# Kernel optimization log

Hardware: AMD Instinct MI355X
Metric: run time of the kernel (lower is better)

Reference implementation:

```python
import jax, jax.numpy as jnp
import numpy as np

N, E, IN_F, H1, F1, H2, F2, OUT_F = 50000, 800000, 128, 4, 32, 1, 64, 2
NEG_SLOPE = 0.2  # PyG GATConv default


def setup_inputs() -> dict:
    key = jax.random.key(0)
    ks = jax.random.split(key, 10)
    p = lambda k, shp: jax.random.normal(k, shp, jnp.float32) * 0.1
    return {
        "x": jax.random.normal(ks[0], (N, IN_F), jnp.float32),
        "edge_index": jax.random.randint(ks[1], (2, E), 0, N),
        "W1": p(ks[2], (IN_F, H1 * F1)),
        "att_s1": p(ks[3], (H1, F1)),
        "att_d1": p(ks[4], (H1, F1)),
        "b1": jnp.zeros((H1 * F1,), jnp.float32),
        "W2": p(ks[5], (H1 * F1, H2 * F2)),
        "att_s2": p(ks[6], (H2, F2)),
        "att_d2": p(ks[7], (H2, F2)),
        "b2": jnp.zeros((F2,), jnp.float32),
        "Wl": p(ks[8], (F2, OUT_F)),
        "bl": jnp.zeros((OUT_F,), jnp.float32),
    }


def _gat_conv(x, src, dst, W, att_s, att_d, bias, concat):
    # PyG GATConv: per-head linear, leaky-relu attention logits,
    # segment-softmax over incoming edges of each dst, scatter-add aggregate.
    n = x.shape[0]
    H, F = att_s.shape
    h = (x @ W).reshape(n, H, F)                        # [N, H, F]
    a_s = jnp.einsum('nhf,hf->nh', h, att_s)            # [N, H]
    a_d = jnp.einsum('nhf,hf->nh', h, att_d)
    logits = jax.nn.leaky_relu(a_s[src] + a_d[dst], NEG_SLOPE)  # [Etot, H]
    m = jax.ops.segment_max(logits, dst, num_segments=n)
    e = jnp.exp(logits - m[dst])
    denom = jax.ops.segment_sum(e, dst, num_segments=n)
    alpha = e / denom[dst]                              # segment softmax
    msg = h[src] * alpha[:, :, None]                    # [Etot, H, F]
    out = jax.ops.segment_sum(msg, dst, num_segments=n)  # [N, H, F]
    out = out.reshape(n, H * F) if concat else out.mean(axis=1)
    return out + bias


def reference(x, edge_index, W1, att_s1, att_d1, b1, W2, att_s2, att_d2, b2, Wl, bl):
    n = x.shape[0]
    loops = jnp.arange(n, dtype=edge_index.dtype)       # add_self_loops=True
    src = jnp.concatenate([edge_index[0], loops])
    dst = jnp.concatenate([edge_index[1], loops])
    h = jax.nn.elu(_gat_conv(x, src, dst, W1, att_s1, att_d1, b1, True))
    h = jax.nn.elu(_gat_conv(h, src, dst, W2, att_s2, att_d2, b2, False))
    pooled = h.sum(axis=0, keepdims=True)               # global_add_pool, batch=0
    out = pooled @ Wl + bl
    return pooled, out
```

## Files before the change

kernel.cpp:

```cpp
#include <hip/hip_runtime.h>

#define N_NODES 50000
#define N_EDGES 800000
#define NB 196
#define P1_BLOCKS 256
#define EPB 3125
#define BH_SIZE (NB * P1_BLOCKS)
#define GEMM_BLOCKS ((N_NODES + 63) / 64)
#define AGG_BLOCKS (N_NODES / 4)
#define EBS_CAP 5120

__device__ __forceinline__ float lrelu(float x) { return fmaxf(x, 0.2f * x); }
__device__ __forceinline__ float elu(float x) { return x > 0.f ? x : __expf(x) - 1.f; }

typedef float f32x2 __attribute__((ext_vector_type(2)));
typedef float f32x4v __attribute__((ext_vector_type(4)));
typedef short bf16x8 __attribute__((ext_vector_type(8)));

__device__ __forceinline__ unsigned f2bf_rn(float x) {
  unsigned u = __float_as_uint(x);
  return (u + 0x7fffu + ((u >> 16) & 1u)) >> 16;
}
__device__ __forceinline__ unsigned pack2bf(float a, float b) {
  return f2bf_rn(a) | (f2bf_rn(b) << 16);
}
__device__ __forceinline__ uint4 pack8bf(const float* v) {
  uint4 o;
  o.x = pack2bf(v[0], v[1]); o.y = pack2bf(v[2], v[3]);
  o.z = pack2bf(v[4], v[5]); o.w = pack2bf(v[6], v[7]);
  return o;
}

__device__ __forceinline__ int block_excl_scan(int v, int* total_out) {
  int lane = threadIdx.x & 63;
  int wid = threadIdx.x >> 6;
  int x = v;
#pragma unroll
  for (int off = 1; off < 64; off <<= 1) {
    int u = __shfl_up(x, off);
    if (lane >= off) x += u;
  }
  __shared__ int wsum[4];
  if (lane == 63) wsum[wid] = x;
  __syncthreads();
  int add = 0;
#pragma unroll
  for (int k = 0; k < 4; ++k)
    if (k < wid) add += wsum[k];
  if (total_out) *total_out = wsum[0] + wsum[1] + wsum[2] + wsum[3];
  return x + add - v;
}

__global__ __launch_bounds__(256) void setup_hist_kernel(
    const int* __restrict__ ei, int* __restrict__ bh,
    const float* __restrict__ W1, const float* __restrict__ atts1, const float* __restrict__ attd1,
    const float* __restrict__ W2, const float* __restrict__ atts2, const float* __restrict__ attd2,
    uint4* __restrict__ Wpk1, uint4* __restrict__ Wpk2, float* __restrict__ pooled) {
  __shared__ int cnt[NB];
  int bid = blockIdx.x;
  if (bid >= 2) {
    for (int t = threadIdx.x; t < NB; t += 256) cnt[t] = 0;
    __syncthreads();
    int start = (bid - 2) * EPB;
    for (int i = start + threadIdx.x; i < start + EPB; i += 256)
      atomicAdd(&cnt[ei[N_EDGES + i] >> 8], 1);
    __syncthreads();
    for (int t = threadIdx.x; t < NB; t += 256)
      bh[t * P1_BLOCKS + (bid - 2)] = cnt[t];
    return;
  }
  if (bid == 0) {
    for (int s = threadIdx.x; s < 4 * 9 * 64; s += 256) {
      int l = s & 63, sf = s >> 6;
      int f = sf % 9, ks = sf / 9;
      int colb = f * 16 + (l & 15);
      int kb = ks * 32 + ((l >> 4) << 3);
      float v[8];
      if (colb < 128) {
#pragma unroll
        for (int j = 0; j < 8; ++j) v[j] = W1[(kb + j) * 128 + colb];
      } else if (colb < 136) {
        int cc = colb - 128;
        const float* at = (cc < 4) ? atts1 : attd1;
        int h = cc & 3;
#pragma unroll
        for (int j = 0; j < 8; ++j) {
          float s2 = 0.f;
          for (int q = 0; q < 32; ++q) s2 += W1[(kb + j) * 128 + h * 32 + q] * at[h * 32 + q];
          v[j] = s2;
        }
      } else {
#pragma unroll
        for (int j = 0; j < 8; ++j) v[j] = 0.f;
      }
      Wpk1[s] = pack8bf(v);
    }
  } else {
    for (int s = threadIdx.x; s < 4 * 5 * 64; s += 256) {
      int l = s & 63, sf = s >> 6;
      int f = sf % 5, ks = sf / 5;
      int colb = f * 16 + (l & 15);
      int kb = ks * 32 + ((l >> 4) << 3);
      float v[8];
      if (colb < 64) {
#pragma unroll
        for (int j = 0; j < 8; ++j) v[j] = W2[(kb + j) * 64 + colb];
      } else if (colb < 66) {
        const float* at = (colb == 64) ? atts2 : attd2;
#pragma unroll
        for (int j = 0; j < 8; ++j) {
          float s2 = 0.f;
          for (int q = 0; q < 64; ++q) s2 += W2[(kb + j) * 64 + q] * at[q];
          v[j] = s2;
        }
      } else {
#pragma unroll
        for (int j = 0; j < 8; ++j) v[j] = 0.f;
      }
      Wpk2[s] = pack8bf(v);
    }
    for (int i = threadIdx.x; i < 64 * 64; i += 256) pooled[i] = 0.f;
  }
}

template <int NF, bool ABF16>
__device__ __forceinline__ void mfma_gemm_body(int bx, const void* __restrict__ Ap,
                                               const uint4* __restrict__ Wpk,
                                               unsigned* __restrict__ Yb,
                                               float* __restrict__ as_out, float* __restrict__ ad_out) {
  __shared__ unsigned short Xs[64 * 136];
  __shared__ uint4 Ws[NF * 64];
  int t = threadIdx.x;
  int rbase = bx * 64;
  if constexpr (ABF16) {
    const uint4* A4 = (const uint4*)Ap;
#pragma unroll
    for (int p = 0; p < 4; ++p) {
      int i = p * 256 + t;
      int row = i >> 4, q = i & 15;
      int gr = rbase + row; if (gr > N_NODES - 1) gr = N_NODES - 1;
      *(uint4*)&Xs[row * 136 + q * 8] = A4[gr * 16 + q];
    }
  } else {
    const float4* A4 = (const float4*)Ap;
#pragma unroll
    for (int p = 0; p < 8; ++p) {
      int i = p * 256 + t;
      int row = i >> 5, q = i & 31;
      int gr = rbase + row; if (gr > N_NODES - 1) gr = N_NODES - 1;
      float4 v = A4[gr * 32 + q];
      *(uint2*)&Xs[row * 136 + q * 4] = make_uint2(pack2bf(v.x, v.y), pack2bf(v.z, v.w));
    }
  }

  int l = t & 63, wv = t >> 6;
  int lc = l & 15, lk = l >> 4;
  f32x4v acc[NF];
#pragma unroll
  for (int f = 0; f < NF; ++f) acc[f] = (f32x4v){0.f, 0.f, 0.f, 0.f};
  const unsigned short* ap = &Xs[(wv * 16 + lc) * 136 + lk * 8];
#pragma unroll
  for (int ks = 0; ks < 4; ++ks) {
    for (int i = t; i < NF * 64; i += 256) Ws[i] = Wpk[ks * NF * 64 + i];
    __syncthreads();
    bf16x8 a = *(const bf16x8*)(ap + ks * 32);
#pragma unroll
    for (int f = 0; f < NF; ++f) {
      bf16x8 b = *(const bf16x8*)&Ws[f * 64 + l];
      acc[f] = __builtin_amdgcn_mfma_f32_16x16x32_bf16(a, b, acc[f], 0, 0, 0);
    }
    if (ks < 3) __syncthreads();
  }

  constexpr int NCF = NF - 1;
#pragma unroll
  for (int reg = 0; reg < 4; ++reg) {
    int row = rbase + wv * 16 + lk * 4 + reg;
    bool rok = row < N_NODES;
    float av = acc[NCF][reg];
    if (rok) {
      if constexpr (NF == 9) {
        if (lc < 4) as_out[row * 4 + lc] = av;
        else if (lc < 8) ad_out[row * 4 + lc - 4] = av;
      } else {
        if (lc == 0) as_out[row] = av;
        else if (lc == 1) ad_out[row] = av;
      }
    }
    unsigned words[NCF];
#pragma unroll
    for (int f = 0; f < NCF; ++f) {
      float v = acc[f][reg];
      float n1 = __shfl_xor(v, 1);
      unsigned pk = (unsigned)__builtin_amdgcn_cvt_pk_fp8_f32(v, n1, 0, false);
      unsigned pk2 = (unsigned)__shfl_xor((int)pk, 2);
      words[f] = (pk & 0xffffu) | (pk2 << 16);
    }
    if (rok && (lc & 3) == 0) {
#pragma unroll
      for (int f = 0; f < NCF; ++f)
        Yb[row * (NCF * 4) + f * 4 + (lc >> 2)] = words[f];
    }
  }
}

__global__ __launch_bounds__(256) void gemm128_scan_kernel(
    const float* __restrict__ x, const uint4* __restrict__ Wpk1,
    unsigned* __restrict__ h1b, float* __restrict__ as1, float* __restrict__ ad1,
    const int* __restrict__ bh, int* __restrict__ bhP, int* __restrict__ blocksum) {
  if (blockIdx.x < GEMM_BLOCKS) {
    mfma_gemm_body<9, false>(blockIdx.x, x, Wpk1, h1b, as1, ad1);
  } else {
    int b = blockIdx.x - GEMM_BLOCKS;
    int g = b * 256 + threadIdx.x;
    int v = bh[g];
    int total;
    int ex = block_excl_scan(v, &total);
    bhP[g] = ex;
    if (threadIdx.x == 0) blocksum[b] = total;
  }
}

__global__ __launch_bounds__(256) void gemm64_kernel(const uint4* __restrict__ h1eb,
                                                     const uint4* __restrict__ Wpk2,
                                                     unsigned* __restrict__ h2b,
                                                     float* __restrict__ as2, float* __restrict__ ad2) {
  mfma_gemm_body<5, true>(blockIdx.x, h1eb, Wpk2, h2b, as2, ad2);
}

__global__ __launch_bounds__(256) void scatter1_kernel(const int* __restrict__ ei, const int* __restrict__ bhP,
                                                       const int* __restrict__ blocksum, unsigned* __restrict__ eb) {
  __shared__ int cur[NB];
  __shared__ int boff[NB];
  int t = threadIdx.x;
  for (int i = t; i < NB; i += 256) cur[i] = 0;
  {
    int v = (t < NB) ? blocksum[t] : 0;
    int ex = block_excl_scan(v, nullptr);
    if (t < NB) boff[t] = ex;
  }
  __syncthreads();
  int start = blockIdx.x * EPB;
  for (int i = start + t; i < start + EPB; i += 256) {
    int dst = ei[N_EDGES + i];
    int src = ei[i];
    int bin = dst >> 8;
    int r = atomicAdd(&cur[bin], 1);
    int idx = bin * P1_BLOCKS + blockIdx.x;
    int pos = bhP[idx] + boff[bin] + r;
    eb[pos] = (unsigned)src | ((unsigned)(dst & 255) << 16);
  }
}

__global__ __launch_bounds__(256) void bucket_csr_kernel(const unsigned* __restrict__ eb,
                                                         const int* __restrict__ blocksum,
                                                         int* __restrict__ rowptrF, int* __restrict__ col) {
  __shared__ unsigned ebs[EBS_CAP];
  __shared__ int cnt[256];
  __shared__ int basel[256];
  __shared__ int cur[256];
  __shared__ int sse[2];
  int b = blockIdx.x;
  int t = threadIdx.x;
  {
    int v = (t < NB) ? blocksum[t] : 0;
    int ex0 = block_excl_scan(v, nullptr);
    if (t == b) sse[0] = ex0;
    if (t == b + 1) sse[1] = ex0;
  }
  cnt[t] = 0;
  cur[t] = 0;
  __syncthreads();
  int start = sse[0];
  int end = (b == NB - 1) ? N_EDGES : sse[1];
  int m = end - start;
  bool fits = (m <= EBS_CAP);
  for (int i = t; i < m; i += 256) {
    unsigned e = eb[start + i];
    if (fits) ebs[i] = e;
    atomicAdd(&cnt[e >> 16], 1);
  }
  __syncthreads();
  int ex = block_excl_scan(cnt[t], nullptr);
  basel[t] = start + ex;
  int g = b * 256 + t;
  if (g < N_NODES) rowptrF[g] = start + ex;
  if (g == N_NODES) rowptrF[N_NODES] = N_EDGES;
  __syncthreads();
  for (int i = t; i < m; i += 256) {
    unsigned e = fits ? ebs[i] : eb[start + i];
    int d8 = e >> 16;
    int r = atomicAdd(&cur[d8], 1);
    col[basel[d8] + r] = (int)(e & 0xffffu);
  }
}

__global__ __launch_bounds__(256) void agg1_kernel(const uint2* __restrict__ h1f8, const int* __restrict__ rowptr,
                                                   const int* __restrict__ col, const float* __restrict__ as1,
                                                   const float* __restrict__ ad1, const float4* __restrict__ b1v,
                                                   uint4* __restrict__ h1eb4) {
  int n = (blockIdx.x * 256 + threadIdx.x) >> 6;
  int lane = threadIdx.x & 63;
  int slot = lane >> 4;
  int fo = lane & 15;
  int h = fo >> 2;
  int beg = rowptr[n], end = rowptr[n + 1];
  float adh = ad1[n * 4 + h];

  f32x2 acc2[4];
#pragma unroll
  for (int j = 0; j < 4; ++j) acc2[j] = (f32x2){0.f, 0.f};
  float esum = 0.f;

#define ACC_EDGE1(E)                                               \
  {                                                                \
    int src = col[E];                                              \
    float a = __expf(lrelu(as1[src * 4 + h] + adh));               \
    esum += a;                                                     \
    f32x2 av = {a, a};                                             \
    uint2 uu = h1f8[src * 16 + fo];                                \
    f32x2 p0 = __builtin_amdgcn_cvt_pk_f32_fp8(uu.x, false);       \
    f32x2 p1 = __builtin_amdgcn_cvt_pk_f32_fp8(uu.x, true);        \
    f32x2 p2 = __builtin_amdgcn_cvt_pk_f32_fp8(uu.y, false);       \
    f32x2 p3 = __builtin_amdgcn_cvt_pk_f32_fp8(uu.y, true);       \
    acc2[0] += av * p0; acc2[1] += av * p1;                        \
    acc2[2] += av * p2; acc2[3] += av * p3;                        \
  }

  int i = beg;
  for (; i + 16 <= end; i += 16) {
#pragma unroll
    for (int u = 0; u < 4; ++u) ACC_EDGE1(i + u * 4 + slot);
  }
  for (; i + 4 <= end; i += 4) ACC_EDGE1(i + slot);
  int rem = end - i;
  if (slot < rem) ACC_EDGE1(i + slot);
#undef ACC_EDGE1
  if (slot == 0) {
    float a = __expf(lrelu(as1[n * 4 + h] + adh));
    esum += a;
    f32x2 av = {a, a};
    uint2 uu = h1f8[n * 16 + fo];
    f32x2 p0 = __builtin_amdgcn_cvt_pk_f32_fp8(uu.x, false);
    f32x2 p1 = __builtin_amdgcn_cvt_pk_f32_fp8(uu.x, true);
    f32x2 p2 = __builtin_amdgcn_cvt_pk_f32_fp8(uu.y, false);
    f32x2 p3 = __builtin_amdgcn_cvt_pk_f32_fp8(uu.y, true);
    acc2[0] += av * p0; acc2[1] += av * p1;
    acc2[2] += av * p2; acc2[3] += av * p3;
  }
#pragma unroll
  for (int j = 0; j < 4; ++j) {
    acc2[j].x += __shfl_xor(acc2[j].x, 16);
    acc2[j].y += __shfl_xor(acc2[j].y, 16);
    acc2[j].x += __shfl_xor(acc2[j].x, 32);
    acc2[j].y += __shfl_xor(acc2[j].y, 32);
  }
  esum += __shfl_xor(esum, 16);
  esum += __shfl_xor(esum, 32);
  if (slot == 0) {
    float dsc = 1.f / esum;
    float4 b0 = b1v[fo * 2], b1 = b1v[fo * 2 + 1];
    float f0 = elu(acc2[0].x * dsc + b0.x), f1 = elu(acc2[0].y * dsc + b0.y);
    float f2 = elu(acc2[1].x * dsc + b0.z), f3 = elu(acc2[1].y * dsc + b0.w);
    float f4 = elu(acc2[2].x * dsc + b1.x), f5 = elu(acc2[2].y * dsc + b1.y);
    float f6 = elu(acc2[3].x * dsc + b1.z), f7 = elu(acc2[3].y * dsc + b1.w);
    uint4 o;
    o.x = pack2bf(f0, f1); o.y = pack2bf(f2, f3);
    o.z = pack2bf(f4, f5); o.w = pack2bf(f6, f7);
    h1eb4[n * 16 + fo] = o;
  }
}

__global__ __launch_bounds__(256) void agg2_kernel(const uint2* __restrict__ h2f8, const int* __restrict__ rowptr,
                                                   const int* __restrict__ col, const float* __restrict__ as2,
                                                   const float* __restrict__ ad2, const float4* __restrict__ b2v,
                                                   float* __restrict__ pooled) {
  __shared__ float red[4][64];
  int n = (blockIdx.x * 256 + threadIdx.x) >> 6;
  int lane = threadIdx.x & 63;
  int wid = threadIdx.x >> 6;
  int slot = lane >> 3;
  int fo = lane & 7;
  int beg = rowptr[n], end = rowptr[n + 1];
  float ad = ad2[n];

  f32x2 acc2[4];
#pragma unroll
  for (int j = 0; j < 4; ++j) acc2[j] = (f32x2){0.f, 0.f};
  float esum = 0.f;

#define ACC_EDGE2(E)                                               \
  {                                                                \
    int src = col[E];                                              \
    float a = __expf(lrelu(as2[src] + ad));                        \
    esum += a;                                                     \
    f32x2 av = {a, a};                                             \
    uint2 uu = h2f8[src * 8 + fo];                                 \
    f32x2 p0 = __builtin_amdgcn_cvt_pk_f32_fp8(uu.x, false);       \
    f32x2 p1 = __builtin_amdgcn_cvt_pk_f32_fp8(uu.x, true);        \
    f32x2 p2 = __builtin_amdgcn_cvt_pk_f32_fp8(uu.y, false);       \
    f32x2 p3 = __builtin_amdgcn_cvt_pk_f32_fp8(uu.y, true);       \
    acc2[0] += av * p0; acc2[1] += av * p1;                        \
    acc2[2] += av * p2; acc2[3] += av * p3;                        \
  }

  int i = beg;
  for (; i + 32 <= end; i += 32) {
#pragma unroll
    for (int u = 0; u < 4; ++u) ACC_EDGE2(i + u * 8 + slot);
  }
  for (; i + 8 <= end; i += 8) ACC_EDGE2(i + slot);
  int rem = end - i;
  if (slot < rem) ACC_EDGE2(i + slot);
#undef ACC_EDGE2
  if (slot == 0) {
    float a = __expf(lrelu(as2[n] + ad));
    esum += a;
    f32x2 av = {a, a};
    uint2 uu = h2f8[n * 8 + fo];
    f32x2 p0 = __builtin_amdgcn_cvt_pk_f32_fp8(uu.x, false);
    f32x2 p1 = __builtin_amdgcn_cvt_pk_f32_fp8(uu.x, true);
    f32x2 p2 = __builtin_amdgcn_cvt_pk_f32_fp8(uu.y, false);
    f32x2 p3 = __builtin_amdgcn_cvt_pk_f32_fp8(uu.y, true);
    acc2[0] += av * p0; acc2[1] += av * p1;
    acc2[2] += av * p2; acc2[3] += av * p3;
  }
#pragma unroll
  for (int j = 0; j < 4; ++j) {
#pragma unroll
    for (int off = 8; off <= 32; off <<= 1) {
      acc2[j].x += __shfl_xor(acc2[j].x, off);
      acc2[j].y += __shfl_xor(acc2[j].y, off);
    }
  }
  esum += __shfl_xor(esum, 8);
  esum += __shfl_xor(esum, 16);
  esum += __shfl_xor(esum, 32);
  if (slot == 0) {
    float dsc = 1.f / esum;
    float4 b0 = b2v[fo * 2], b1 = b2v[fo * 2 + 1];
    red[wid][fo * 8 + 0] = elu(acc2[0].x * dsc + b0.x);
    red[wid][fo * 8 + 1] = elu(acc2[0].y * dsc + b0.y);
    red[wid][fo * 8 + 2] = elu(acc2[1].x * dsc + b0.z);
    red[wid][fo * 8 + 3] = elu(acc2[1].y * dsc + b0.w);
    red[wid][fo * 8 + 4] = elu(acc2[2].x * dsc + b1.x);
    red[wid][fo * 8 + 5] = elu(acc2[2].y * dsc + b1.y);
    red[wid][fo * 8 + 6] = elu(acc2[3].x * dsc + b1.z);
    red[wid][fo * 8 + 7] = elu(acc2[3].y * dsc + b1.w);
  }
  __syncthreads();
  if (threadIdx.x < 64) {
    float sum = red[0][threadIdx.x] + red[1][threadIdx.x] + red[2][threadIdx.x] + red[3][threadIdx.x];
    atomicAdd(&pooled[(blockIdx.x & 63) * 64 + threadIdx.x], sum);
  }
}

__global__ void final_kernel(const float* __restrict__ pooledS, const float* __restrict__ Wl,
                             const float* __restrict__ bl, float* __restrict__ out) {
  __shared__ float p[64];
  int t = threadIdx.x;
  float v = 0.f;
  for (int k = 0; k < 64; ++k) v += pooledS[k * 64 + t];
  p[t] = v;
  out[t] = v;
  __syncthreads();
  if (t < 2) {
    float s = bl[t];
    for (int k = 0; k < 64; ++k) s += p[k] * Wl[k * 2 + t];
    out[64 + t] = s;
  }
}

extern "C" void kernel_launch(void* const* d_in, const int* in_sizes, int n_in,
                              void* d_out, int out_size, void* d_ws, size_t ws_size,
                              hipStream_t stream) {
  (void)in_sizes; (void)n_in; (void)out_size; (void)ws_size;
  const float* x     = (const float*)d_in[0];
  const int*   ei    = (const int*)d_in[1];
  const float* W1    = (const float*)d_in[2];
  const float* atts1 = (const float*)d_in[3];
  const float* attd1 = (const float*)d_in[4];
  const float* b1    = (const float*)d_in[5];
  const float* W2    = (const float*)d_in[6];
  const float* atts2 = (const float*)d_in[7];
  const float* attd2 = (const float*)d_in[8];
  const float* b2    = (const float*)d_in[9];
  const float* Wl    = (const float*)d_in[10];
  const float* bl    = (const float*)d_in[11];
  float* out = (float*)d_out;

  char* w = (char*)d_ws;
  unsigned* h1b  = (unsigned*)w; w += (size_t)N_NODES * 128;
  unsigned* h1eb = (unsigned*)w; w += (size_t)N_NODES * 128 * 2;
  unsigned* h2b  = (unsigned*)w; w += (size_t)N_NODES * 64;
  float* as1  = (float*)w; w += (size_t)N_NODES * 16;
  float* ad1  = (float*)w; w += (size_t)N_NODES * 16;
  float* as2  = (float*)w; w += (size_t)N_NODES * 4;
  float* ad2  = (float*)w; w += (size_t)N_NODES * 4;
  float* pooled = (float*)w; w += 64 * 64 * 4;
  uint4* Wpk1 = (uint4*)w; w += 4 * 9 * 64 * 16;
  uint4* Wpk2 = (uint4*)w; w += 4 * 5 * 64 * 16;
  int* rowptrF = (int*)w; w += (size_t)(N_NODES + 1) * 4 + 12;
  int* col    = (int*)w; w += (size_t)N_EDGES * 4;
  unsigned* eb = (unsigned*)w; w += (size_t)N_EDGES * 4;
  int* bh     = (int*)w; w += (size_t)BH_SIZE * 4;
  int* bhP    = (int*)w; w += (size_t)BH_SIZE * 4;
  int* blocksum = (int*)w; w += 256 * 4;

  setup_hist_kernel<<<258, 256, 0, stream>>>(ei, bh, W1, atts1, attd1, W2, atts2, attd2,
                                             Wpk1, Wpk2, pooled);
  gemm128_scan_kernel<<<GEMM_BLOCKS + NB, 256, 0, stream>>>(x, Wpk1, h1b, as1, ad1, bh, bhP, blocksum);
  scatter1_kernel<<<P1_BLOCKS, 256, 0, stream>>>(ei, bhP, blocksum, eb);
  bucket_csr_kernel<<<NB, 256, 0, stream>>>(eb, blocksum, rowptrF, col);
  agg1_kernel<<<AGG_BLOCKS, 256, 0, stream>>>((const uint2*)h1b, rowptrF, col, as1, ad1,
                                              (const float4*)b1, (uint4*)h1eb);
  gemm64_kernel<<<GEMM_BLOCKS, 256, 0, stream>>>((const uint4*)h1eb, Wpk2, h2b, as2, ad2);
  agg2_kernel<<<AGG_BLOCKS, 256, 0, stream>>>((const uint2*)h2b, rowptrF, col, as2, ad2,
                                              (const float4*)b2, pooled);
  final_kernel<<<1, 64, 0, stream>>>(pooled, Wl, bl, out);
}
```

Measured before the change: 204.9 us.

## Fold histogram scan into scatter blocks and final reduction into agg2 last-block

Removes the separate scan pass and scatter kernel: each scatter block, co-launched with the first GEMM, computes its own per-bin prefix by reading its bin's histogram row directly, and block 0 publishes global bin offsets for the CSR build. The final pooling/linear kernel is replaced by a last-block-done pattern in agg2 using an atomic counter. This cuts two kernel launches and the bhP round trip. In exchange every scatter block redundantly reads the whole histogram, and the last-block pattern relies on atomic ordering.

```diff
diff --git a/kernel.cpp b/kernel.cpp
--- a/kernel.cpp
+++ b/kernel.cpp
@@ -5,7 +5,6 @@
 #define NB 196
 #define P1_BLOCKS 256
 #define EPB 3125
-#define BH_SIZE (NB * P1_BLOCKS)
 #define GEMM_BLOCKS ((N_NODES + 63) / 64)
 #define AGG_BLOCKS (N_NODES / 4)
 #define EBS_CAP 5120
@@ -55,7 +54,8 @@
     const int* __restrict__ ei, int* __restrict__ bh,
     const float* __restrict__ W1, const float* __restrict__ atts1, const float* __restrict__ attd1,
     const float* __restrict__ W2, const float* __restrict__ atts2, const float* __restrict__ attd2,
-    uint4* __restrict__ Wpk1, uint4* __restrict__ Wpk2, float* __restrict__ pooled) {
+    uint4* __restrict__ Wpk1, uint4* __restrict__ Wpk2, float* __restrict__ pooled,
+    int* __restrict__ done) {
   __shared__ int cnt[NB];
   int bid = blockIdx.x;
   if (bid >= 2) {
@@ -120,6 +120,7 @@
       Wpk2[s] = pack8bf(v);
     }
     for (int i = threadIdx.x; i < 64 * 64; i += 256) pooled[i] = 0.f;
+    if (threadIdx.x == 0) *done = 0;
   }
 }
 
@@ -204,20 +205,60 @@
   }
 }
 
-__global__ __launch_bounds__(256) void gemm128_scan_kernel(
+__device__ __forceinline__ void scatter_body(int bid, const int* __restrict__ ei,
+                                             const int* __restrict__ bh,
+                                             unsigned* __restrict__ eb, int* __restrict__ gboff) {
+  __shared__ int pref[NB];
+  __shared__ int boff[NB];
+  __shared__ int cur[NB];
+  int t = threadIdx.x;
+  int tot = 0;
+  if (t < NB) {
+    const uint4* bh4 = (const uint4*)(bh + t * P1_BLOCKS);
+    int pf = 0, tt = 0;
+    for (int g = 0; g < P1_BLOCKS / 4; ++g) {
+      uint4 u = bh4[g];
+      int s4 = (int)(u.x + u.y + u.z + u.w);
+      tt += s4;
+      int j = g * 4;
+      if (j + 4 <= bid) {
+        pf += s4;
+      } else if (j < bid) {
+        pf += (j + 0 < bid ? (int)u.x : 0) + (j + 1 < bid ? (int)u.y : 0) +
+              (j + 2 < bid ? (int)u.z : 0) + (j + 3 < bid ? (int)u.w : 0);
+      }
+    }
+    pref[t] = pf;
+    cur[t] = 0;
+    tot = tt;
+  }
+  int ex = block_excl_scan((t < NB) ? tot : 0, nullptr);
+  if (t < NB) boff[t] = ex;
+  if (bid == 0) {
+    if (t < NB) gboff[t] = ex;
+    if (t == 0) gboff[NB] = N_EDGES;
+  }
+  __syncthreads();
+  int start = bid * EPB;
+  for (int i = start + t; i < start + EPB; i += 256) {
+    int dst = ei[N_EDGES + i];
+    int src = ei[i];
+    int bin = dst >> 8;
+    int r = atomicAdd(&cur[bin], 1);
+    int pos = pref[bin] + boff[bin] + r;
+    eb[pos] = (unsigned)src | ((unsigned)(dst & 255) << 16);
+  }
+}
+
+__global__ __launch_bounds__(256) void gemm128_scatter_kernel(
     const float* __restrict__ x, const uint4* __restrict__ Wpk1,
     unsigned* __restrict__ h1b, float* __restrict__ as1, float* __restrict__ ad1,
-    const int* __restrict__ bh, int* __restrict__ bhP, int* __restrict__ blocksum) {
+    const int* __restrict__ ei, const int* __restrict__ bh,
+    unsigned* __restrict__ eb, int* __restrict__ gboff) {
   if (blockIdx.x < GEMM_BLOCKS) {
     mfma_gemm_body<9, false>(blockIdx.x, x, Wpk1, h1b, as1, ad1);
   } else {
-    int b = blockIdx.x - GEMM_BLOCKS;
-    int g = b * 256 + threadIdx.x;
-    int v = bh[g];
-    int total;
-    int ex = block_excl_scan(v, &total);
-    bhP[g] = ex;
-    if (threadIdx.x == 0) blocksum[b] = total;
+    scatter_body(blockIdx.x - GEMM_BLOCKS, ei, bh, eb, gboff);
   }
 }
 
@@ -228,51 +269,20 @@
   mfma_gemm_body<5, true>(blockIdx.x, h1eb, Wpk2, h2b, as2, ad2);
 }
 
-__global__ __launch_bounds__(256) void scatter1_kernel(const int* __restrict__ ei, const int* __restrict__ bhP,
-                                                       const int* __restrict__ blocksum, unsigned* __restrict__ eb) {
-  __shared__ int cur[NB];
-  __shared__ int boff[NB];
-  int t = threadIdx.x;
-  for (int i = t; i < NB; i += 256) cur[i] = 0;
-  {
-    int v = (t < NB) ? blocksum[t] : 0;
-    int ex = block_excl_scan(v, nullptr);
-    if (t < NB) boff[t] = ex;
-  }
-  __syncthreads();
-  int start = blockIdx.x * EPB;
-  for (int i = start + t; i < start + EPB; i += 256) {
-    int dst = ei[N_EDGES + i];
-    int src = ei[i];
-    int bin = dst >> 8;
-    int r = atomicAdd(&cur[bin], 1);
-    int idx = bin * P1_BLOCKS + blockIdx.x;
-    int pos = bhP[idx] + boff[bin] + r;
-    eb[pos] = (unsigned)src | ((unsigned)(dst & 255) << 16);
-  }
-}
-
 __global__ __launch_bounds__(256) void bucket_csr_kernel(const unsigned* __restrict__ eb,
-                                                         const int* __restrict__ blocksum,
+                                                         const int* __restrict__ gboff,
                                                          int* __restrict__ rowptrF, int* __restrict__ col) {
   __shared__ unsigned ebs[EBS_CAP];
   __shared__ int cnt[256];
   __shared__ int basel[256];
   __shared__ int cur[256];
-  __shared__ int sse[2];
   int b = blockIdx.x;
   int t = threadIdx.x;
-  {
-    int v = (t < NB) ? blocksum[t] : 0;
-    int ex0 = block_excl_scan(v, nullptr);
-    if (t == b) sse[0] = ex0;
-    if (t == b + 1) sse[1] = ex0;
-  }
   cnt[t] = 0;
   cur[t] = 0;
   __syncthreads();
-  int start = sse[0];
-  int end = (b == NB - 1) ? N_EDGES : sse[1];
+  int start = gboff[b];
+  int end = gboff[b + 1];
   int m = end - start;
   bool fits = (m <= EBS_CAP);
   for (int i = t; i < m; i += 256) {
@@ -374,8 +384,12 @@
 __global__ __launch_bounds__(256) void agg2_kernel(const uint2* __restrict__ h2f8, const int* __restrict__ rowptr,
                                                    const int* __restrict__ col, const float* __restrict__ as2,
                                                    const float* __restrict__ ad2, const float4* __restrict__ b2v,
-                                                   float* __restrict__ pooled) {
+                                                   float* __restrict__ pooled, const float* __restrict__ Wl,
+                                                   const float* __restrict__ bl, float* __restrict__ out,
+                                                   int* __restrict__ done) {
   __shared__ float red[4][64];
+  __shared__ float pfin[64];
+  __shared__ int lastf;
   int n = (blockIdx.x * 256 + threadIdx.x) >> 6;
   int lane = threadIdx.x & 63;
   int wid = threadIdx.x >> 6;
@@ -449,25 +463,30 @@
     red[wid][fo * 8 + 7] = elu(acc2[3].y * dsc + b1.w);
   }
   __syncthreads();
+  float old = 0.f;
   if (threadIdx.x < 64) {
     float sum = red[0][threadIdx.x] + red[1][threadIdx.x] + red[2][threadIdx.x] + red[3][threadIdx.x];
-    atomicAdd(&pooled[(blockIdx.x & 63) * 64 + threadIdx.x], sum);
-  }
-}
-
-__global__ void final_kernel(const float* __restrict__ pooledS, const float* __restrict__ Wl,
-                             const float* __restrict__ bl, float* __restrict__ out) {
-  __shared__ float p[64];
-  int t = threadIdx.x;
-  float v = 0.f;
-  for (int k = 0; k < 64; ++k) v += pooledS[k * 64 + t];
-  p[t] = v;
-  out[t] = v;
-  __syncthreads();
-  if (t < 2) {
-    float s = bl[t];
-    for (int k = 0; k < 64; ++k) s += p[k] * Wl[k * 2 + t];
-    out[64 + t] = s;
+    old = atomicAdd(&pooled[(blockIdx.x & 63) * 64 + threadIdx.x], sum);
+  }
+  asm volatile("s_waitcnt vmcnt(0)" :: "v"(old) : "memory");
+  if (threadIdx.x == 0)
+    lastf = (atomicAdd(done, 1) == AGG_BLOCKS - 1);
+  __syncthreads();
+  if (lastf) {
+    int t = threadIdx.x;
+    if (t < 64) {
+      float v = 0.f;
+      for (int k = 0; k < 64; ++k)
+        v += __hip_atomic_load(&pooled[k * 64 + t], __ATOMIC_RELAXED, __HIP_MEMORY_SCOPE_AGENT);
+      pfin[t] = v;
+      out[t] = v;
+    }
+    __syncthreads();
+    if (t < 2) {
+      float s = bl[t];
+      for (int k = 0; k < 64; ++k) s += pfin[k] * Wl[k * 2 + t];
+      out[64 + t] = s;
+    }
   }
 }
 
@@ -503,19 +522,18 @@
   int* rowptrF = (int*)w; w += (size_t)(N_NODES + 1) * 4 + 12;
   int* col    = (int*)w; w += (size_t)N_EDGES * 4;
   unsigned* eb = (unsigned*)w; w += (size_t)N_EDGES * 4;
-  int* bh     = (int*)w; w += (size_t)BH_SIZE * 4;
-  int* bhP    = (int*)w; w += (size_t)BH_SIZE * 4;
-  int* blocksum = (int*)w; w += 256 * 4;
+  int* bh     = (int*)w; w += (size_t)NB * P1_BLOCKS * 4;
+  int* gboff  = (int*)w; w += 800;
+  int* done   = (int*)w; w += 16;
 
   setup_hist_kernel<<<258, 256, 0, stream>>>(ei, bh, W1, atts1, attd1, W2, atts2, attd2,
-                                             Wpk1, Wpk2, pooled);
-  gemm128_scan_kernel<<<GEMM_BLOCKS + NB, 256, 0, stream>>>(x, Wpk1, h1b, as1, ad1, bh, bhP, blocksum);
-  scatter1_kernel<<<P1_BLOCKS, 256, 0, stream>>>(ei, bhP, blocksum, eb);
-  bucket_csr_kernel<<<NB, 256, 0, stream>>>(eb, blocksum, rowptrF, col);
+                                             Wpk1, Wpk2, pooled, done);
+  gemm128_scatter_kernel<<<GEMM_BLOCKS + P1_BLOCKS, 256, 0, stream>>>(
+      x, Wpk1, h1b, as1, ad1, ei, bh, eb, gboff);
+  bucket_csr_kernel<<<NB, 256, 0, stream>>>(eb, gboff, rowptrF, col);
   agg1_kernel<<<AGG_BLOCKS, 256, 0, stream>>>((const uint2*)h1b, rowptrF, col, as1, ad1,
                                               (const float4*)b1, (uint4*)h1eb);
   gemm64_kernel<<<GEMM_BLOCKS, 256, 0, stream>>>((const uint4*)h1eb, Wpk2, h2b, as2, ad2);
   agg2_kernel<<<AGG_BLOCKS, 256, 0, stream>>>((const uint2*)h2b, rowptrF, col, as2, ad2,
-                                              (const float4*)b2, pooled);
-  final_kernel<<<1, 64, 0, stream>>>(pooled, Wl, bl, out);
-}
+                                              (const float4*)b2, pooled, Wl, bl, out, done);
+}
```

New measurement: 333.3 us. +62.7%, slower.

## Replace two-level bucketed CSR build with per-node atomic count/scan/scatter

Applied to the files above, without the earlier changes.

Replaces the bucket histogram, bucket scan, bucketed scatter and per-bucket local sort with a direct per-destination global atomic histogram, a single-block scan over all nodes, and an atomic-cursor scatter into col. This removes one kernel launch and the intermediate eb buffer, and zeroes the counts and pooled buffer with a memset. In exchange it adds heavy global atomic contention, a serial single-block scan of 50k counts, and a nondeterministic edge order within each row.

```diff
diff --git a/kernel.cpp b/kernel.cpp
--- a/kernel.cpp
+++ b/kernel.cpp
@@ -2,13 +2,11 @@
 
 #define N_NODES 50000
 #define N_EDGES 800000
-#define NB 196
 #define P1_BLOCKS 256
 #define EPB 3125
-#define BH_SIZE (NB * P1_BLOCKS)
 #define GEMM_BLOCKS ((N_NODES + 63) / 64)
 #define AGG_BLOCKS (N_NODES / 4)
-#define EBS_CAP 5120
+#define SCAN_CHUNK 196
 
 __device__ __forceinline__ float lrelu(float x) { return fmaxf(x, 0.2f * x); }
 __device__ __forceinline__ float elu(float x) { return x > 0.f ? x : __expf(x) - 1.f; }
@@ -52,21 +50,15 @@
 }
 
 __global__ __launch_bounds__(256) void setup_hist_kernel(
-    const int* __restrict__ ei, int* __restrict__ bh,
+    const int* __restrict__ ei, int* __restrict__ cnt,
     const float* __restrict__ W1, const float* __restrict__ atts1, const float* __restrict__ attd1,
     const float* __restrict__ W2, const float* __restrict__ atts2, const float* __restrict__ attd2,
-    uint4* __restrict__ Wpk1, uint4* __restrict__ Wpk2, float* __restrict__ pooled) {
-  __shared__ int cnt[NB];
+    uint4* __restrict__ Wpk1, uint4* __restrict__ Wpk2) {
   int bid = blockIdx.x;
   if (bid >= 2) {
-    for (int t = threadIdx.x; t < NB; t += 256) cnt[t] = 0;
-    __syncthreads();
     int start = (bid - 2) * EPB;
     for (int i = start + threadIdx.x; i < start + EPB; i += 256)
-      atomicAdd(&cnt[ei[N_EDGES + i] >> 8], 1);
-    __syncthreads();
-    for (int t = threadIdx.x; t < NB; t += 256)
-      bh[t * P1_BLOCKS + (bid - 2)] = cnt[t];
+      atomicAdd(&cnt[ei[N_EDGES + i]], 1);
     return;
   }
   if (bid == 0) {
@@ -119,7 +111,6 @@
       }
       Wpk2[s] = pack8bf(v);
     }
-    for (int i = threadIdx.x; i < 64 * 64; i += 256) pooled[i] = 0.f;
   }
 }
 
@@ -207,17 +198,25 @@
 __global__ __launch_bounds__(256) void gemm128_scan_kernel(
     const float* __restrict__ x, const uint4* __restrict__ Wpk1,
     unsigned* __restrict__ h1b, float* __restrict__ as1, float* __restrict__ ad1,
-    const int* __restrict__ bh, int* __restrict__ bhP, int* __restrict__ blocksum) {
+    const int* __restrict__ cnt, int* __restrict__ segstart, int* __restrict__ cursor) {
   if (blockIdx.x < GEMM_BLOCKS) {
     mfma_gemm_body<9, false>(blockIdx.x, x, Wpk1, h1b, as1, ad1);
   } else {
-    int b = blockIdx.x - GEMM_BLOCKS;
-    int g = b * 256 + threadIdx.x;
-    int v = bh[g];
-    int total;
-    int ex = block_excl_scan(v, &total);
-    bhP[g] = ex;
-    if (threadIdx.x == 0) blocksum[b] = total;
+    int t = threadIdx.x;
+    int s = 0;
+    for (int i = 0; i < SCAN_CHUNK; ++i) {
+      int n = i * 256 + t;
+      if (n < N_NODES) s += cnt[n];
+    }
+    int running = block_excl_scan(s, nullptr);
+    for (int i = 0; i < SCAN_CHUNK; ++i) {
+      int n = i * 256 + t;
+      if (n < N_NODES) {
+        segstart[n] = running;
+        cursor[n] = running;
+        running += cnt[n];
+      }
+    }
   }
 }
 
@@ -228,74 +227,21 @@
   mfma_gemm_body<5, true>(blockIdx.x, h1eb, Wpk2, h2b, as2, ad2);
 }
 
-__global__ __launch_bounds__(256) void scatter1_kernel(const int* __restrict__ ei, const int* __restrict__ bhP,
-                                                       const int* __restrict__ blocksum, unsigned* __restrict__ eb) {
-  __shared__ int cur[NB];
-  __shared__ int boff[NB];
-  int t = threadIdx.x;
-  for (int i = t; i < NB; i += 256) cur[i] = 0;
-  {
-    int v = (t < NB) ? blocksum[t] : 0;
-    int ex = block_excl_scan(v, nullptr);
-    if (t < NB) boff[t] = ex;
-  }
-  __syncthreads();
+__global__ __launch_bounds__(256) void scatter_kernel(const int* __restrict__ ei,
+                                                      int* __restrict__ cursor,
+                                                      int* __restrict__ col) {
   int start = blockIdx.x * EPB;
-  for (int i = start + t; i < start + EPB; i += 256) {
+  for (int i = start + threadIdx.x; i < start + EPB; i += 256) {
     int dst = ei[N_EDGES + i];
     int src = ei[i];
-    int bin = dst >> 8;
-    int r = atomicAdd(&cur[bin], 1);
-    int idx = bin * P1_BLOCKS + blockIdx.x;
-    int pos = bhP[idx] + boff[bin] + r;
-    eb[pos] = (unsigned)src | ((unsigned)(dst & 255) << 16);
-  }
-}
-
-__global__ __launch_bounds__(256) void bucket_csr_kernel(const unsigned* __restrict__ eb,
-                                                         const int* __restrict__ blocksum,
-                                                         int* __restrict__ rowptrF, int* __restrict__ col) {
-  __shared__ unsigned ebs[EBS_CAP];
-  __shared__ int cnt[256];
-  __shared__ int basel[256];
-  __shared__ int cur[256];
-  __shared__ int sse[2];
-  int b = blockIdx.x;
-  int t = threadIdx.x;
-  {
-    int v = (t < NB) ? blocksum[t] : 0;
-    int ex0 = block_excl_scan(v, nullptr);
-    if (t == b) sse[0] = ex0;
-    if (t == b + 1) sse[1] = ex0;
-  }
-  cnt[t] = 0;
-  cur[t] = 0;
-  __syncthreads();
-  int start = sse[0];
-  int end = (b == NB - 1) ? N_EDGES : sse[1];
-  int m = end - start;
-  bool fits = (m <= EBS_CAP);
-  for (int i = t; i < m; i += 256) {
-    unsigned e = eb[start + i];
-    if (fits) ebs[i] = e;
-    atomicAdd(&cnt[e >> 16], 1);
-  }
-  __syncthreads();
-  int ex = block_excl_scan(cnt[t], nullptr);
-  basel[t] = start + ex;
-  int g = b * 256 + t;
-  if (g < N_NODES) rowptrF[g] = start + ex;
-  if (g == N_NODES) rowptrF[N_NODES] = N_EDGES;
-  __syncthreads();
-  for (int i = t; i < m; i += 256) {
-    unsigned e = fits ? ebs[i] : eb[start + i];
-    int d8 = e >> 16;
-    int r = atomicAdd(&cur[d8], 1);
-    col[basel[d8] + r] = (int)(e & 0xffffu);
-  }
-}
-
-__global__ __launch_bounds__(256) void agg1_kernel(const uint2* __restrict__ h1f8, const int* __restrict__ rowptr,
+    int pos = atomicAdd(&cursor[dst], 1);
+    col[pos] = src;
+  }
+}
+
+__global__ __launch_bounds__(256) void agg1_kernel(const uint2* __restrict__ h1f8,
+                                                   const int* __restrict__ segstart,
+                                                   const int* __restrict__ cnt,
                                                    const int* __restrict__ col, const float* __restrict__ as1,
                                                    const float* __restrict__ ad1, const float4* __restrict__ b1v,
                                                    uint4* __restrict__ h1eb4) {
@@ -304,7 +250,8 @@
   int slot = lane >> 4;
   int fo = lane & 15;
   int h = fo >> 2;
-  int beg = rowptr[n], end = rowptr[n + 1];
+  int beg = segstart[n];
+  int end = beg + cnt[n];
   float adh = ad1[n * 4 + h];
 
   f32x2 acc2[4];
@@ -371,7 +318,9 @@
   }
 }
 
-__global__ __launch_bounds__(256) void agg2_kernel(const uint2* __restrict__ h2f8, const int* __restrict__ rowptr,
+__global__ __launch_bounds__(256) void agg2_kernel(const uint2* __restrict__ h2f8,
+                                                   const int* __restrict__ segstart,
+                                                   const int* __restrict__ cnt,
                                                    const int* __restrict__ col, const float* __restrict__ as2,
                                                    const float* __restrict__ ad2, const float4* __restrict__ b2v,
                                                    float* __restrict__ pooled) {
@@ -381,7 +330,8 @@
   int wid = threadIdx.x >> 6;
   int slot = lane >> 3;
   int fo = lane & 7;
-  int beg = rowptr[n], end = rowptr[n + 1];
+  int beg = segstart[n];
+  int end = beg + cnt[n];
   float ad = ad2[n];
 
   f32x2 acc2[4];
@@ -490,6 +440,8 @@
   float* out = (float*)d_out;
 
   char* w = (char*)d_ws;
+  int* cnt    = (int*)w; w += (size_t)N_NODES * 4;
+  float* pooled = (float*)w; w += 64 * 64 * 4;
   unsigned* h1b  = (unsigned*)w; w += (size_t)N_NODES * 128;
   unsigned* h1eb = (unsigned*)w; w += (size_t)N_NODES * 128 * 2;
   unsigned* h2b  = (unsigned*)w; w += (size_t)N_NODES * 64;
@@ -497,25 +449,23 @@
   float* ad1  = (float*)w; w += (size_t)N_NODES * 16;
   float* as2  = (float*)w; w += (size_t)N_NODES * 4;
   float* ad2  = (float*)w; w += (size_t)N_NODES * 4;
-  float* pooled = (float*)w; w += 64 * 64 * 4;
   uint4* Wpk1 = (uint4*)w; w += 4 * 9 * 64 * 16;
   uint4* Wpk2 = (uint4*)w; w += 4 * 5 * 64 * 16;
-  int* rowptrF = (int*)w; w += (size_t)(N_NODES + 1) * 4 + 12;
+  int* segstart = (int*)w; w += (size_t)N_NODES * 4;
+  int* cursor   = (int*)w; w += (size_t)N_NODES * 4;
   int* col    = (int*)w; w += (size_t)N_EDGES * 4;
-  unsigned* eb = (unsigned*)w; w += (size_t)N_EDGES * 4;
-  int* bh     = (int*)w; w += (size_t)BH_SIZE * 4;
-  int* bhP    = (int*)w; w += (size_t)BH_SIZE * 4;
-  int* blocksum = (int*)w; w += 256 * 4;
-
-  setup_hist_kernel<<<258, 256, 0, stream>>>(ei, bh, W1, atts1, attd1, W2, atts2, attd2,
-                                             Wpk1, Wpk2, pooled);
-  gemm128_scan_kernel<<<GEMM_BLOCKS + NB, 256, 0, stream>>>(x, Wpk1, h1b, as1, ad1, bh, bhP, blocksum);
-  scatter1_kernel<<<P1_BLOCKS, 256, 0, stream>>>(ei, bhP, blocksum, eb);
-  bucket_csr_kernel<<<NB, 256, 0, stream>>>(eb, blocksum, rowptrF, col);
-  agg1_kernel<<<AGG_BLOCKS, 256, 0, stream>>>((const uint2*)h1b, rowptrF, col, as1, ad1,
+
+  (void)hipMemsetAsync(cnt, 0, (size_t)N_NODES * 4 + 64 * 64 * 4, stream);
+
+  setup_hist_kernel<<<258, 256, 0, stream>>>(ei, cnt, W1, atts1, attd1, W2, atts2, attd2,
+                                             Wpk1, Wpk2);
+  gemm128_scan_kernel<<<GEMM_BLOCKS + 1, 256, 0, stream>>>(x, Wpk1, h1b, as1, ad1,
+                                                           cnt, segstart, cursor);
+  scatter_kernel<<<P1_BLOCKS, 256, 0, stream>>>(ei, cursor, col);
+  agg1_kernel<<<AGG_BLOCKS, 256, 0, stream>>>((const uint2*)h1b, segstart, cnt, col, as1, ad1,
                                               (const float4*)b1, (uint4*)h1eb);
   gemm64_kernel<<<GEMM_BLOCKS, 256, 0, stream>>>((const uint4*)h1eb, Wpk2, h2b, as2, ad2);
-  agg2_kernel<<<AGG_BLOCKS, 256, 0, stream>>>((const uint2*)h2b, rowptrF, col, as2, ad2,
+  agg2_kernel<<<AGG_BLOCKS, 256, 0, stream>>>((const uint2*)h2b, segstart, cnt, col, as2, ad2,
                                               (const float4*)b2, pooled);
   final_kernel<<<1, 64, 0, stream>>>(pooled, Wl, bl, out);
 }
```

Result: slower. 316.8 us (+54.6%).

## Fuse layer-1 aggregation with layer-2 GEMM through shared memory

Applied to the files above, without the earlier changes.

Merges the agg1 and gemm64 kernels. Each block now aggregates 64 nodes (16 per wave, one after another) into a bf16 tile in LDS, then runs the MFMA projection for layer 2 directly from that tile. This removes the global h1eb round trip (write plus read of about 12.8 MB) and one kernel launch. In exchange, parallelism falls from 12500 blocks of 4 nodes each to 782 blocks where each wave walks 16 nodes serially, so latency hiding for the gather could get worse.

```diff
diff --git a/kernel.cpp b/kernel.cpp
--- a/kernel.cpp
+++ b/kernel.cpp
@@ -221,13 +221,6 @@
   }
 }
 
-__global__ __launch_bounds__(256) void gemm64_kernel(const uint4* __restrict__ h1eb,
-                                                     const uint4* __restrict__ Wpk2,
-                                                     unsigned* __restrict__ h2b,
-                                                     float* __restrict__ as2, float* __restrict__ ad2) {
-  mfma_gemm_body<5, true>(blockIdx.x, h1eb, Wpk2, h2b, as2, ad2);
-}
-
 __global__ __launch_bounds__(256) void scatter1_kernel(const int* __restrict__ ei, const int* __restrict__ bhP,
                                                        const int* __restrict__ blocksum, unsigned* __restrict__ eb) {
   __shared__ int cur[NB];
@@ -295,79 +288,130 @@
   }
 }
 
-__global__ __launch_bounds__(256) void agg1_kernel(const uint2* __restrict__ h1f8, const int* __restrict__ rowptr,
-                                                   const int* __restrict__ col, const float* __restrict__ as1,
-                                                   const float* __restrict__ ad1, const float4* __restrict__ b1v,
-                                                   uint4* __restrict__ h1eb4) {
-  int n = (blockIdx.x * 256 + threadIdx.x) >> 6;
-  int lane = threadIdx.x & 63;
-  int slot = lane >> 4;
-  int fo = lane & 15;
+__global__ __launch_bounds__(256) void agg1_gemm64_kernel(
+    const uint2* __restrict__ h1f8, const int* __restrict__ rowptr, const int* __restrict__ col,
+    const float* __restrict__ as1, const float* __restrict__ ad1, const float4* __restrict__ b1v,
+    const uint4* __restrict__ Wpk2, unsigned* __restrict__ h2b,
+    float* __restrict__ as2, float* __restrict__ ad2) {
+  __shared__ unsigned short Xs[64 * 136];
+  __shared__ uint4 Ws[5 * 64];
+  int t = threadIdx.x;
+  int rbase = blockIdx.x * 64;
+  int l = t & 63, wv = t >> 6;
+  int slot = l >> 4;
+  int fo = l & 15;
   int h = fo >> 2;
-  int beg = rowptr[n], end = rowptr[n + 1];
-  float adh = ad1[n * 4 + h];
-
-  f32x2 acc2[4];
-#pragma unroll
-  for (int j = 0; j < 4; ++j) acc2[j] = (f32x2){0.f, 0.f};
-  float esum = 0.f;
+
+  for (int it = 0; it < 16; ++it) {
+    int n = rbase + wv * 16 + it;
+    if (n < N_NODES) {
+      int beg = rowptr[n], end = rowptr[n + 1];
+      float adh = ad1[n * 4 + h];
+      f32x2 acc2[4];
+#pragma unroll
+      for (int j = 0; j < 4; ++j) acc2[j] = (f32x2){0.f, 0.f};
+      float esum = 0.f;
 
 #define ACC_EDGE1(E)                                               \
-  {                                                                \
-    int src = col[E];                                              \
-    float a = __expf(lrelu(as1[src * 4 + h] + adh));               \
-    esum += a;                                                     \
-    f32x2 av = {a, a};                                             \
-    uint2 uu = h1f8[src * 16 + fo];                                \
-    f32x2 p0 = __builtin_amdgcn_cvt_pk_f32_fp8(uu.x, false);       \
-    f32x2 p1 = __builtin_amdgcn_cvt_pk_f32_fp8(uu.x, true);        \
-    f32x2 p2 = __builtin_amdgcn_cvt_pk_f32_fp8(uu.y, false);       \
-    f32x2 p3 = __builtin_amdgcn_cvt_pk_f32_fp8(uu.y, true);       \
-    acc2[0] += av * p0; acc2[1] += av * p1;                        \
-    acc2[2] += av * p2; acc2[3] += av * p3;                        \
-  }
-
-  int i = beg;
-  for (; i + 16 <= end; i += 16) {
-#pragma unroll
-    for (int u = 0; u < 4; ++u) ACC_EDGE1(i + u * 4 + slot);
-  }
-  for (; i + 4 <= end; i += 4) ACC_EDGE1(i + slot);
-  int rem = end - i;
-  if (slot < rem) ACC_EDGE1(i + slot);
+      {                                                            \
+        int src = col[E];                                          \
+        float a = __expf(lrelu(as1[src * 4 + h] + adh));           \
+        esum += a;                                                 \
+        f32x2 av = {a, a};                                         \
+        uint2 uu = h1f8[src * 16 + fo];                            \
+        f32x2 p0 = __builtin_amdgcn_cvt_pk_f32_fp8(uu.x, false);   \
+        f32x2 p1 = __builtin_amdgcn_cvt_pk_f32_fp8(uu.x, true);    \
+        f32x2 p2 = __builtin_amdgcn_cvt_pk_f32_fp8(uu.y, false);   \
+        f32x2 p3 = __builtin_amdgcn_cvt_pk_f32_fp8(uu.y, true);    \
+        acc2[0] += av * p0; acc2[1] += av * p1;                    \
+        acc2[2] += av * p2; acc2[3] += av * p3;                    \
+      }
+
+      int i = beg;
+      for (; i + 16 <= end; i += 16) {
+#pragma unroll
+        for (int u = 0; u < 4; ++u) ACC_EDGE1(i + u * 4 + slot);
+      }
+      for (; i + 4 <= end; i += 4) ACC_EDGE1(i + slot);
+      int rem = end - i;
+      if (slot < rem) ACC_EDGE1(i + slot);
+      if (slot == 0) {
+        float a = __expf(lrelu(as1[n * 4 + h] + adh));
+        esum += a;
+        f32x2 av = {a, a};
+        uint2 uu = h1f8[n * 16 + fo];
+        f32x2 p0 = __builtin_amdgcn_cvt_pk_f32_fp8(uu.x, false);
+        f32x2 p1 = __builtin_amdgcn_cvt_pk_f32_fp8(uu.x, true);
+        f32x2 p2 = __builtin_amdgcn_cvt_pk_f32_fp8(uu.y, false);
+        f32x2 p3 = __builtin_amdgcn_cvt_pk_f32_fp8(uu.y, true);
+        acc2[0] += av * p0; acc2[1] += av * p1;
+        acc2[2] += av * p2; acc2[3] += av * p3;
+      }
 #undef ACC_EDGE1
-  if (slot == 0) {
-    float a = __expf(lrelu(as1[n * 4 + h] + adh));
-    esum += a;
-    f32x2 av = {a, a};
-    uint2 uu = h1f8[n * 16 + fo];
-    f32x2 p0 = __builtin_amdgcn_cvt_pk_f32_fp8(uu.x, false);
-    f32x2 p1 = __builtin_amdgcn_cvt_pk_f32_fp8(uu.x, true);
-    f32x2 p2 = __builtin_amdgcn_cvt_pk_f32_fp8(uu.y, false);
-    f32x2 p3 = __builtin_amdgcn_cvt_pk_f32_fp8(uu.y, true);
-    acc2[0] += av * p0; acc2[1] += av * p1;
-    acc2[2] += av * p2; acc2[3] += av * p3;
-  }
-#pragma unroll
-  for (int j = 0; j < 4; ++j) {
-    acc2[j].x += __shfl_xor(acc2[j].x, 16);
-    acc2[j].y += __shfl_xor(acc2[j].y, 16);
-    acc2[j].x += __shfl_xor(acc2[j].x, 32);
-    acc2[j].y += __shfl_xor(acc2[j].y, 32);
-  }
-  esum += __shfl_xor(esum, 16);
-  esum += __shfl_xor(esum, 32);
-  if (slot == 0) {
-    float dsc = 1.f / esum;
-    float4 b0 = b1v[fo * 2], b1 = b1v[fo * 2 + 1];
-    float f0 = elu(acc2[0].x * dsc + b0.x), f1 = elu(acc2[0].y * dsc + b0.y);
-    float f2 = elu(acc2[1].x * dsc + b0.z), f3 = elu(acc2[1].y * dsc + b0.w);
-    float f4 = elu(acc2[2].x * dsc + b1.x), f5 = elu(acc2[2].y * dsc + b1.y);
-    float f6 = elu(acc2[3].x * dsc + b1.z), f7 = elu(acc2[3].y * dsc + b1.w);
-    uint4 o;
-    o.x = pack2bf(f0, f1); o.y = pack2bf(f2, f3);
-    o.z = pack2bf(f4, f5); o.w = pack2bf(f6, f7);
-    h1eb4[n * 16 + fo] = o;
+#pragma unroll
+      for (int j = 0; j < 4; ++j) {
+        acc2[j].x += __shfl_xor(acc2[j].x, 16);
+        acc2[j].y += __shfl_xor(acc2[j].y, 16);
+        acc2[j].x += __shfl_xor(acc2[j].x, 32);
+        acc2[j].y += __shfl_xor(acc2[j].y, 32);
+      }
+      esum += __shfl_xor(esum, 16);
+      esum += __shfl_xor(esum, 32);
+      if (slot == 0) {
+        float dsc = 1.f / esum;
+        float4 b0 = b1v[fo * 2], b1 = b1v[fo * 2 + 1];
+        float f0 = elu(acc2[0].x * dsc + b0.x), f1 = elu(acc2[0].y * dsc + b0.y);
+        float f2 = elu(acc2[1].x * dsc + b0.z), f3 = elu(acc2[1].y * dsc + b0.w);
+        float f4 = elu(acc2[2].x * dsc + b1.x), f5 = elu(acc2[2].y * dsc + b1.y);
+        float f6 = elu(acc2[3].x * dsc + b1.z), f7 = elu(acc2[3].y * dsc + b1.w);
+        uint4 o;
+        o.x = pack2bf(f0, f1); o.y = pack2bf(f2, f3);
+        o.z = pack2bf(f4, f5); o.w = pack2bf(f6, f7);
+        *(uint4*)&Xs[(wv * 16 + it) * 136 + fo * 8] = o;
+      }
+    }
+  }
+
+  int lc = l & 15, lk = l >> 4;
+  f32x4v acc[5];
+#pragma unroll
+  for (int f = 0; f < 5; ++f) acc[f] = (f32x4v){0.f, 0.f, 0.f, 0.f};
+  const unsigned short* ap = &Xs[(wv * 16 + lc) * 136 + lk * 8];
+#pragma unroll
+  for (int ks = 0; ks < 4; ++ks) {
+    for (int i = t; i < 5 * 64; i += 256) Ws[i] = Wpk2[ks * 5 * 64 + i];
+    __syncthreads();
+    bf16x8 a = *(const bf16x8*)(ap + ks * 32);
+#pragma unroll
+    for (int f = 0; f < 5; ++f) {
+      bf16x8 b = *(const bf16x8*)&Ws[f * 64 + l];
+      acc[f] = __builtin_amdgcn_mfma_f32_16x16x32_bf16(a, b, acc[f], 0, 0, 0);
+    }
+    if (ks < 3) __syncthreads();
+  }
+#pragma unroll
+  for (int reg = 0; reg < 4; ++reg) {
+    int row = rbase + wv * 16 + lk * 4 + reg;
+    bool rok = row < N_NODES;
+    float av = acc[4][reg];
+    if (rok) {
+      if (lc == 0) as2[row] = av;
+      else if (lc == 1) ad2[row] = av;
+    }
+    unsigned words[4];
+#pragma unroll
+    for (int f = 0; f < 4; ++f) {
+      float v = acc[f][reg];
+      float n1 = __shfl_xor(v, 1);
+      unsigned pk = (unsigned)__builtin_amdgcn_cvt_pk_fp8_f32(v, n1, 0, false);
+      unsigned pk2 = (unsigned)__shfl_xor((int)pk, 2);
+      words[f] = (pk & 0xffffu) | (pk2 << 16);
+    }
+    if (rok && (lc & 3) == 0) {
+#pragma unroll
+      for (int f = 0; f < 4; ++f)
+        h2b[row * 16 + f * 4 + (lc >> 2)] = words[f];
+    }
   }
 }
 
@@ -491,7 +535,6 @@
 
   char* w = (char*)d_ws;
   unsigned* h1b  = (unsigned*)w; w += (size_t)N_NODES * 128;
-  unsigned* h1eb = (unsigned*)w; w += (size_t)N_NODES * 128 * 2;
   unsigned* h2b  = (unsigned*)w; w += (size_t)N_NODES * 64;
   float* as1  = (float*)w; w += (size_t)N_NODES * 16;
   float* ad1  = (float*)w; w += (size_t)N_NODES * 16;
@@ -512,9 +555,8 @@
   gemm128_scan_kernel<<<GEMM_BLOCKS + NB, 256, 0, stream>>>(x, Wpk1, h1b, as1, ad1, bh, bhP, blocksum);
   scatter1_kernel<<<P1_BLOCKS, 256, 0, stream>>>(ei, bhP, blocksum, eb);
   bucket_csr_kernel<<<NB, 256, 0, stream>>>(eb, blocksum, rowptrF, col);
-  agg1_kernel<<<AGG_BLOCKS, 256, 0, stream>>>((const uint2*)h1b, rowptrF, col, as1, ad1,
-                                              (const float4*)b1, (uint4*)h1eb);
-  gemm64_kernel<<<GEMM_BLOCKS, 256, 0, stream>>>((const uint4*)h1eb, Wpk2, h2b, as2, ad2);
+  agg1_gemm64_kernel<<<GEMM_BLOCKS, 256, 0, stream>>>((const uint2*)h1b, rowptrF, col, as1, ad1,
+                                                      (const float4*)b1, Wpk2, h2b, as2, ad2);
   agg2_kernel<<<AGG_BLOCKS, 256, 0, stream>>>((const uint2*)h2b, rowptrF, col, as2, ad2,
                                               (const float4*)b2, pooled);
   final_kernel<<<1, 64, 0, stream>>>(pooled, Wl, bl, out);
```

New measurement: 227.1 us. 1.11x slower.
